# Optimization experiments

Hardware: AMD Instinct MI355X
Metric: run time of the kernel (lower is better)

The kernel has to match this reference:

```python
import jax, jax.numpy as jnp
import numpy as np

B, M, N, D, H = 4, 8, 128, 32, 64
SMALL_V = 1e-8


def setup_inputs() -> dict:
    key = jax.random.key(0)
    ks = jax.random.split(key, 12)
    s = 0.05
    x = jax.random.normal(ks[0], (B, M, N, D), jnp.float32)
    sizes = jax.random.randint(ks[1], (B,), N // 2, N + 1)
    valid = (jnp.arange(N)[None, :] < sizes[:, None]).astype(jnp.float32)  # [B,N]
    x = x * valid[:, None, :, None]  # zero out padded items
    return {
        "x": x,
        "x_size": sizes.astype(jnp.float32),
        "W1a": jax.random.normal(ks[2], (D, 2 * D), jnp.float32) * s,
        "b1a": jax.random.normal(ks[3], (2 * D,), jnp.float32) * s,
        "W1b": jax.random.normal(ks[4], (2 * D, D), jnp.float32) * s,
        "b1b": jax.random.normal(ks[5], (D,), jnp.float32) * s,
        "W2a": jax.random.normal(ks[6], (D, 2 * D), jnp.float32) * s,
        "b2a": jax.random.normal(ks[7], (2 * D,), jnp.float32) * s,
        "W2b": jax.random.normal(ks[8], (2 * D, H), jnp.float32) * s,
        "b2b": jax.random.normal(ks[9], (H,), jnp.float32) * s,
        "w3": jax.random.normal(ks[10], (H,), jnp.float32) * s,
        "b3": jax.random.normal(ks[11], (1,), jnp.float32) * s,
    }


def _item_mask(x):
    # 1.0 where the item's feature row has any nonzero entry, else 0.0. [...,N,1]
    return jnp.any(x != 0, axis=-1, keepdims=True).astype(x.dtype)


def _set_norm(x, x_size):
    # layer_normalization with is_set_norm=True: normalize over (N*D) per set,
    # dividing by the true valid size x_size*D and masking padded items.
    b, m, n, d = x.shape
    mask = jnp.broadcast_to(_item_mask(x), x.shape).reshape(b, m, n * d)
    xr = x.reshape(b, m, n * d)
    denom = x_size[:, None] * d  # [B,1] -> broadcasts over nSet
    mean = jnp.sum(xr, axis=-1) / denom  # [B,M]
    diff = xr - mean[..., None]
    std = jnp.sqrt(jnp.sum(diff * diff * mask, axis=-1) / denom)  # [B,M]
    out = diff / (std[..., None] + SMALL_V) * mask
    return out.reshape(b, m, n, d)


def reference(x, x_size, W1a, b1a, W1b, b1b, W2a, b2a, W2b, b2b, w3, b3):
    mask = _item_mask(x)  # [B,M,N,1]
    x_orig = x
    xn = _set_norm(x, x_size) * mask  # [B,M,N,D]
    # MLP1 (rank-4 -> masked by its own input's item mask)
    m1 = _item_mask(xn)
    x1 = (jnp.matmul(jax.nn.gelu(jnp.matmul(xn, W1a) + b1a), W1b) + b1b) * m1
    # pairwise differences: x_diff[b,m,i,j,:] = x1[b,m,i,:] - xn[b,m,j,:]
    x_diff = x1[:, :, :, None, :] - xn[:, :, None, :, :]  # [B,M,N,N,D]
    # MLP2 (rank-5 -> no mask, is_SoftMax=0)
    e = jnp.matmul(jax.nn.gelu(jnp.matmul(x_diff, W2a) + b2a), W2b) + b2b  # [B,M,N,N,H]
    # aggregation: out[b,m,j,h,d] = sum_i e[b,m,i,j,h] * x1[b,m,i,d]
    agg = jnp.einsum('bmijh,bmid->bmjhd', e, x1)
    # MLP3_linear: Dense(1) over H, then squeeze
    out = jnp.einsum('bmjhd,h->bmjd', agg, w3) + b3[0]
    out = (out + x_orig) * mask
    return out
```

## Files before the change

### kernel.cpp

```cpp
#include <hip/hip_runtime.h>

#define BMC 32
#define NNC 128
#define DDC 32
#define KKC 64
constexpr int ND = NNC * DDC;
constexpr int NK = NNC * KKC;
#define SMALLV 1e-8f

__device__ __forceinline__ float gelu_f(float v) {
    float v2 = v * v;
    float p  = fmaf(0.1029432f, v2, 2.3022082f);
    float e  = __builtin_amdgcn_exp2f(v * p);
    float r  = __builtin_amdgcn_rcpf(e + 1.0f);
    return fmaf(-v, r, v);
}

__global__ __launch_bounds__(256) void mlp_kernel(
    const float* __restrict__ x, const float* __restrict__ x_size,
    const float* __restrict__ W1a, const float* __restrict__ b1a,
    const float* __restrict__ W1b, const float* __restrict__ b1b,
    const float* __restrict__ W2a, const float* __restrict__ b2a,
    const float* __restrict__ W2b, const float* __restrict__ b2b,
    const float* __restrict__ w3,
    float* __restrict__ x1g, float* __restrict__ A1g, float* __restrict__ A2t,
    float* __restrict__ v2g, float* __restrict__ c3g)
{
    __shared__ float sW1a[DDC * KKC];
    __shared__ float sW1b[KKC * DDC];
    __shared__ float sW2a[DDC * KKC];
    __shared__ float sXn[8 * DDC];
    __shared__ float sH[8 * KKC];
    __shared__ float sX1[8 * DDC];
    __shared__ float sB1a[KKC], sB2a[KKC], sB1b[DDC];
    __shared__ float sAny[NNC];
    __shared__ float sRed[4];

    const int t  = threadIdx.x;
    const int bm = blockIdx.x >> 4;
    const int nt = blockIdx.x & 15;
    const int n0 = nt * 8;
    const int w  = t >> 6;

    {
        const float4* a4 = (const float4*)W1a;
        const float4* b4 = (const float4*)W1b;
        const float4* c4 = (const float4*)W2a;
        float4* sa = (float4*)sW1a; float4* sb = (float4*)sW1b; float4* sc = (float4*)sW2a;
        sa[t] = a4[t]; sa[t + 256] = a4[t + 256];
        sb[t] = b4[t]; sb[t + 256] = b4[t + 256];
        sc[t] = c4[t]; sc[t + 256] = c4[t + 256];
    }
    if (t < KKC) { sB1a[t] = b1a[t]; sB2a[t] = b2a[t]; }
    if (t < DDC) { sB1b[t] = b1b[t]; }
    if (t < NNC) sAny[t] = 0.f;
    __syncthreads();

    const float4* xs4 = (const float4*)(x + (size_t)bm * ND);
    float4 v4[4];
    float lsum = 0.f;
    #pragma unroll
    for (int s = 0; s < 4; ++s) {
        int f = t + s * 256;
        float4 q = xs4[f];
        v4[s] = q;
        lsum += q.x + q.y + q.z + q.w;
        if (q.x != 0.f || q.y != 0.f || q.z != 0.f || q.w != 0.f) sAny[f >> 3] = 1.f;
    }
    #pragma unroll
    for (int off = 32; off; off >>= 1) lsum += __shfl_xor(lsum, off);
    if ((t & 63) == 0) sRed[w] = lsum;
    __syncthreads();
    const float denom = x_size[bm >> 3] * (float)DDC;
    const float mean  = (sRed[0] + sRed[1] + sRed[2] + sRed[3]) / denom;

    float lsq = 0.f;
    #pragma unroll
    for (int s = 0; s < 4; ++s) {
        int f = t + s * 256;
        float mk = sAny[f >> 3];
        float dx = v4[s].x - mean, dy = v4[s].y - mean;
        float dz = v4[s].z - mean, dw = v4[s].w - mean;
        lsq += mk * (dx * dx + dy * dy + dz * dz + dw * dw);
    }
    #pragma unroll
    for (int off = 32; off; off >>= 1) lsq += __shfl_xor(lsq, off);
    __syncthreads();
    if ((t & 63) == 0) sRed[w] = lsq;
    __syncthreads();
    const float sq  = sRed[0] + sRed[1] + sRed[2] + sRed[3];
    const float inv = 1.f / (sqrtf(sq / denom) + SMALLV);

    {
        float xv = x[(size_t)bm * ND + n0 * DDC + t];
        sXn[t] = (xv - mean) * inv * sAny[n0 + (t >> 5)];
    }
    __syncthreads();

    const int k = t & 63;

    #pragma unroll
    for (int r = 0; r < 2; ++r) {
        int n = w + r * 4;
        const float* xr = &sXn[n * DDC];
        float acc = sB1a[k];
        #pragma unroll
        for (int d = 0; d < DDC; ++d) acc = fmaf(xr[d], sW1a[d * KKC + k], acc);
        sH[n * KKC + k] = gelu_f(acc);
    }
    __syncthreads();

    {
        const int d2 = t & 31;
        const int n  = t >> 5;
        const float* hr = &sH[n * KKC];
        float acc = sB1b[d2];
        #pragma unroll
        for (int q = 0; q < KKC; ++q) acc = fmaf(hr[q], sW1b[q * DDC + d2], acc);
        float val = acc * sAny[n0 + n];
        sX1[n * DDC + d2] = val;
        x1g[(size_t)bm * ND + (n0 + n) * DDC + d2] = val;
    }
    __syncthreads();

    #pragma unroll
    for (int r = 0; r < 2; ++r) {
        int n = w + r * 4;
        const float* x1r = &sX1[n * DDC];
        const float* xnr = &sXn[n * DDC];
        float a1 = sB2a[k], a2 = 0.f;
        #pragma unroll
        for (int d = 0; d < DDC; ++d) {
            a1 = fmaf(x1r[d], sW2a[d * KKC + k], a1);
            a2 = fmaf(xnr[d], sW2a[d * KKC + k], a2);
        }
        A1g[(size_t)bm * NK + (n0 + n) * KKC + k] = a1;
        A2t[(size_t)bm * NK + k * NNC + (n0 + n)] = a2;
    }

    if (blockIdx.x == 0) {
        int kk = t >> 2, hq = t & 3;
        float p = 0.f;
        #pragma unroll
        for (int h = 0; h < 16; ++h)
            p = fmaf(W2b[kk * KKC + hq * 16 + h], w3[hq * 16 + h], p);
        __syncthreads();
        sH[t] = p;
        __syncthreads();
        if (hq == 0) v2g[kk] = sH[t] + sH[t + 1] + sH[t + 2] + sH[t + 3];
        if (t < 64) {
            float q = b2b[t] * w3[t];
            #pragma unroll
            for (int off = 32; off; off >>= 1) q += __shfl_xor(q, off);
            if (t == 0) c3g[0] = q;
        }
    }
}

__global__ __launch_bounds__(256) void pair_kernel(
    const float* __restrict__ x_size,
    const float* __restrict__ A1g, const float* __restrict__ A2t,
    const float* __restrict__ x1g, const float* __restrict__ v2g,
    const float* __restrict__ c3g, float* __restrict__ partial)
{
    __shared__ float sA2[KKC * 64];
    __shared__ float sA1[8 * KKC];
    __shared__ float sX1[8 * DDC];
    __shared__ float sS[8 * 64];
    __shared__ float sV2[KKC];

    const int t    = threadIdx.x;
    const int bm   = blockIdx.x >> 5;
    const int jg   = (blockIdx.x >> 4) & 1;
    const int ig   = blockIdx.x & 15;

    const int iN = (int)(x_size[bm >> 3] + 0.5f);
    if (ig * 8 >= iN || jg * 64 >= iN) return;

    const int wv   = t >> 6;
    const int lane = t & 63;

    {
        const float* A2b = A2t + (size_t)bm * NK + jg * 64;
        float4* s4 = (float4*)sA2;
        #pragma unroll
        for (int s = 0; s < 4; ++s) {
            int idx = t + s * 256;
            int k = idx >> 4, f = idx & 15;
            s4[idx] = *(const float4*)(A2b + k * NNC + f * 4);
        }
    }
    {
        const float2* a1s = (const float2*)(A1g + (size_t)bm * NK + ig * 8 * KKC);
        ((float2*)sA1)[t] = a1s[t];
        sX1[t] = x1g[(size_t)bm * ND + ig * 8 * DDC + t];
        if (t < KKC) sV2[t] = v2g[t];
    }
    const float c3 = c3g[0];
    __syncthreads();

    {
        const int i0 = wv * 2, i1 = i0 + 1;
        float S0 = c3, S1 = c3;
        #pragma unroll 8
        for (int k = 0; k < KKC; ++k) {
            float a2v = sA2[k * 64 + lane];
            float vk  = sV2[k];
            float a10 = sA1[i0 * KKC + k];
            float a11 = sA1[i1 * KKC + k];
            S0 = fmaf(gelu_f(a10 - a2v), vk, S0);
            S1 = fmaf(gelu_f(a11 - a2v), vk, S1);
        }
        sS[i0 * 64 + lane] = S0;
        sS[i1 * 64 + lane] = S1;
    }
    __syncthreads();

    {
        const int j  = t >> 2;
        const int dq = t & 3;
        float acc[8];
        #pragma unroll
        for (int d = 0; d < 8; ++d) acc[d] = 0.f;
        #pragma unroll
        for (int i = 0; i < 8; ++i) {
            float Sv = sS[i * 64 + j];
            const float4* xf = (const float4*)&sX1[i * DDC + dq * 8];
            float4 xa = xf[0], xb = xf[1];
            acc[0] = fmaf(Sv, xa.x, acc[0]);
            acc[1] = fmaf(Sv, xa.y, acc[1]);
            acc[2] = fmaf(Sv, xa.z, acc[2]);
            acc[3] = fmaf(Sv, xa.w, acc[3]);
            acc[4] = fmaf(Sv, xb.x, acc[4]);
            acc[5] = fmaf(Sv, xb.y, acc[5]);
            acc[6] = fmaf(Sv, xb.z, acc[6]);
            acc[7] = fmaf(Sv, xb.w, acc[7]);
        }
        float* pb = partial + ((size_t)((bm * 2 + jg) * 16 + ig)) * 2048 + t * 8;
        ((float4*)pb)[0] = make_float4(acc[0], acc[1], acc[2], acc[3]);
        ((float4*)pb)[1] = make_float4(acc[4], acc[5], acc[6], acc[7]);
    }
}

__global__ __launch_bounds__(256) void final_kernel(
    const float* __restrict__ x, const float* __restrict__ x_size,
    const float* __restrict__ b3,
    const float* __restrict__ partial, float* __restrict__ out)
{
    const int gid = blockIdx.x * 256 + threadIdx.x;
    const int bm  = gid >> 12;
    const int rem = gid & 4095;
    float xv = x[gid];
    unsigned long long bal = __ballot(xv != 0.f);
    int lane = threadIdx.x & 63;
    unsigned long long half = (lane < 32) ? (bal & 0xFFFFFFFFull) : (bal >> 32);
    if (half == 0ull) { out[gid] = 0.f; return; }

    const int iN  = (int)(x_size[bm >> 3] + 0.5f);
    const int nig = (iN + 7) >> 3;
    const int jgp = rem >> 11;
    const size_t pb = ((size_t)((bm * 2 + jgp) * 16)) * 2048 + (rem & 2047);
    float sum = 0.f;
    for (int ig = 0; ig < nig; ++ig) sum += partial[pb + (size_t)ig * 2048];
    out[gid] = sum + b3[0] + xv;
}

extern "C" void kernel_launch(void* const* d_in, const int* in_sizes, int n_in,
                              void* d_out, int out_size, void* d_ws, size_t ws_size,
                              hipStream_t stream) {
    const float* x      = (const float*)d_in[0];
    const float* x_size = (const float*)d_in[1];
    const float* W1a    = (const float*)d_in[2];
    const float* b1a    = (const float*)d_in[3];
    const float* W1b    = (const float*)d_in[4];
    const float* b1b    = (const float*)d_in[5];
    const float* W2a    = (const float*)d_in[6];
    const float* b2a    = (const float*)d_in[7];
    const float* W2b    = (const float*)d_in[8];
    const float* b2b    = (const float*)d_in[9];
    const float* w3     = (const float*)d_in[10];
    const float* b3     = (const float*)d_in[11];
    float* out = (float*)d_out;

    float* ws      = (float*)d_ws;
    float* x1g     = ws;
    float* A1g     = x1g + (size_t)BMC * ND;
    float* A2t     = A1g + (size_t)BMC * NK;
    float* v2g     = A2t + (size_t)BMC * NK;
    float* c3g     = v2g + KKC;
    float* partial = c3g + 64;

    mlp_kernel<<<BMC * 16, 256, 0, stream>>>(x, x_size,
        W1a, b1a, W1b, b1b, W2a, b2a, W2b, b2b, w3,
        x1g, A1g, A2t, v2g, c3g);
    pair_kernel<<<BMC * 32, 256, 0, stream>>>(x_size, A1g, A2t, x1g, v2g, c3g, partial);
    final_kernel<<<512, 256, 0, stream>>>(x, x_size, b3, partial, out);
}
```

Baseline: 104.0 us.

## Fuse final reduction into pair kernel via atomics and register-cache A2 tiles

Removes the separate final reduction kernel: the MLP kernel now seeds the output with x+b3 (zero for padded rows), and the pair kernel atomically adds its per-i-group contributions straight into the output. The pair kernel also handles 16 source items per block, caches each thread's A2 column in registers and computes four rows per wave with vectorized shared loads. This removes a launch and the partial buffer round trip, at the cost of global atomics and higher register pressure. The padding mask now comes from x_size instead of nonzero rows.

New measurement: 122.7 us. 1.18x slower.

```diff
diff --git a/kernel.cpp b/kernel.cpp
--- a/kernel.cpp
+++ b/kernel.cpp
@@ -22,9 +22,9 @@
     const float* __restrict__ W1b, const float* __restrict__ b1b,
     const float* __restrict__ W2a, const float* __restrict__ b2a,
     const float* __restrict__ W2b, const float* __restrict__ b2b,
-    const float* __restrict__ w3,
+    const float* __restrict__ w3, const float* __restrict__ b3,
     float* __restrict__ x1g, float* __restrict__ A1g, float* __restrict__ A2t,
-    float* __restrict__ v2g, float* __restrict__ c3g)
+    float* __restrict__ v2g, float* __restrict__ c3g, float* __restrict__ out)
 {
     __shared__ float sW1a[DDC * KKC];
     __shared__ float sW1b[KKC * DDC];
@@ -71,7 +71,9 @@
     for (int off = 32; off; off >>= 1) lsum += __shfl_xor(lsum, off);
     if ((t & 63) == 0) sRed[w] = lsum;
     __syncthreads();
-    const float denom = x_size[bm >> 3] * (float)DDC;
+    const float xsz   = x_size[bm >> 3];
+    const float denom = xsz * (float)DDC;
+    const int   iN    = (int)(xsz + 0.5f);
     const float mean  = (sRed[0] + sRed[1] + sRed[2] + sRed[3]) / denom;
 
     float lsq = 0.f;
@@ -93,7 +95,9 @@
 
     {
         float xv = x[(size_t)bm * ND + n0 * DDC + t];
-        sXn[t] = (xv - mean) * inv * sAny[n0 + (t >> 5)];
+        int  jr  = n0 + (t >> 5);
+        sXn[t] = (xv - mean) * inv * sAny[jr];
+        out[(size_t)bm * ND + n0 * DDC + t] = (jr < iN) ? xv + b3[0] : 0.f;
     }
     __syncthreads();
 
@@ -161,21 +165,21 @@
     const float* __restrict__ x_size,
     const float* __restrict__ A1g, const float* __restrict__ A2t,
     const float* __restrict__ x1g, const float* __restrict__ v2g,
-    const float* __restrict__ c3g, float* __restrict__ partial)
+    const float* __restrict__ c3g, float* __restrict__ out)
 {
     __shared__ float sA2[KKC * 64];
-    __shared__ float sA1[8 * KKC];
-    __shared__ float sX1[8 * DDC];
-    __shared__ float sS[8 * 64];
+    __shared__ float sA1[16 * KKC];
+    __shared__ float sX1[16 * DDC];
+    __shared__ float sS[16 * 64];
     __shared__ float sV2[KKC];
 
     const int t    = threadIdx.x;
-    const int bm   = blockIdx.x >> 5;
-    const int jg   = (blockIdx.x >> 4) & 1;
-    const int ig   = blockIdx.x & 15;
+    const int bm   = blockIdx.x >> 4;
+    const int jg   = (blockIdx.x >> 3) & 1;
+    const int ig   = blockIdx.x & 7;
 
     const int iN = (int)(x_size[bm >> 3] + 0.5f);
-    if (ig * 8 >= iN || jg * 64 >= iN) return;
+    if (ig * 16 >= iN || jg * 64 >= iN) return;
 
     const int wv   = t >> 6;
     const int lane = t & 63;
@@ -190,29 +194,53 @@
             s4[idx] = *(const float4*)(A2b + k * NNC + f * 4);
         }
     }
-    {
-        const float2* a1s = (const float2*)(A1g + (size_t)bm * NK + ig * 8 * KKC);
-        ((float2*)sA1)[t] = a1s[t];
-        sX1[t] = x1g[(size_t)bm * ND + ig * 8 * DDC + t];
-        if (t < KKC) sV2[t] = v2g[t];
-    }
+    ((float4*)sA1)[t] = ((const float4*)(A1g + (size_t)bm * NK + ig * 16 * KKC))[t];
+    ((float2*)sX1)[t] = ((const float2*)(x1g + (size_t)bm * ND + ig * 16 * DDC))[t];
+    if (t < KKC) sV2[t] = v2g[t];
     const float c3 = c3g[0];
     __syncthreads();
 
-    {
-        const int i0 = wv * 2, i1 = i0 + 1;
-        float S0 = c3, S1 = c3;
-        #pragma unroll 8
-        for (int k = 0; k < KKC; ++k) {
-            float a2v = sA2[k * 64 + lane];
-            float vk  = sV2[k];
-            float a10 = sA1[i0 * KKC + k];
-            float a11 = sA1[i1 * KKC + k];
-            S0 = fmaf(gelu_f(a10 - a2v), vk, S0);
-            S1 = fmaf(gelu_f(a11 - a2v), vk, S1);
-        }
-        sS[i0 * 64 + lane] = S0;
-        sS[i1 * 64 + lane] = S1;
+    float a2r[KKC];
+    #pragma unroll
+    for (int q = 0; q < KKC; ++q) a2r[q] = sA2[q * 64 + lane];
+
+    {
+        const float4* a1f0 = (const float4*)&sA1[(wv * 4 + 0) * KKC];
+        const float4* a1f1 = (const float4*)&sA1[(wv * 4 + 1) * KKC];
+        const float4* a1f2 = (const float4*)&sA1[(wv * 4 + 2) * KKC];
+        const float4* a1f3 = (const float4*)&sA1[(wv * 4 + 3) * KKC];
+        const float4* v2f  = (const float4*)sV2;
+        float S0 = c3, S1 = c3, S2 = c3, S3 = c3;
+        #pragma unroll 4
+        for (int k4 = 0; k4 < 16; ++k4) {
+            float4 vk = v2f[k4];
+            float4 a0 = a1f0[k4];
+            float4 a1 = a1f1[k4];
+            float4 a2 = a1f2[k4];
+            float4 a3 = a1f3[k4];
+            const int kb = k4 * 4;
+            float b0 = a2r[kb + 0], b1 = a2r[kb + 1], b2 = a2r[kb + 2], b3v = a2r[kb + 3];
+            S0 = fmaf(gelu_f(a0.x - b0), vk.x, S0);
+            S1 = fmaf(gelu_f(a1.x - b0), vk.x, S1);
+            S2 = fmaf(gelu_f(a2.x - b0), vk.x, S2);
+            S3 = fmaf(gelu_f(a3.x - b0), vk.x, S3);
+            S0 = fmaf(gelu_f(a0.y - b1), vk.y, S0);
+            S1 = fmaf(gelu_f(a1.y - b1), vk.y, S1);
+            S2 = fmaf(gelu_f(a2.y - b1), vk.y, S2);
+            S3 = fmaf(gelu_f(a3.y - b1), vk.y, S3);
+            S0 = fmaf(gelu_f(a0.z - b2), vk.z, S0);
+            S1 = fmaf(gelu_f(a1.z - b2), vk.z, S1);
+            S2 = fmaf(gelu_f(a2.z - b2), vk.z, S2);
+            S3 = fmaf(gelu_f(a3.z - b2), vk.z, S3);
+            S0 = fmaf(gelu_f(a0.w - b3v), vk.w, S0);
+            S1 = fmaf(gelu_f(a1.w - b3v), vk.w, S1);
+            S2 = fmaf(gelu_f(a2.w - b3v), vk.w, S2);
+            S3 = fmaf(gelu_f(a3.w - b3v), vk.w, S3);
+        }
+        sS[(wv * 4 + 0) * 64 + lane] = S0;
+        sS[(wv * 4 + 1) * 64 + lane] = S1;
+        sS[(wv * 4 + 2) * 64 + lane] = S2;
+        sS[(wv * 4 + 3) * 64 + lane] = S3;
     }
     __syncthreads();
 
@@ -223,7 +251,7 @@
         #pragma unroll
         for (int d = 0; d < 8; ++d) acc[d] = 0.f;
         #pragma unroll
-        for (int i = 0; i < 8; ++i) {
+        for (int i = 0; i < 16; ++i) {
             float Sv = sS[i * 64 + j];
             const float4* xf = (const float4*)&sX1[i * DDC + dq * 8];
             float4 xa = xf[0], xb = xf[1];
@@ -236,33 +264,13 @@
             acc[6] = fmaf(Sv, xb.z, acc[6]);
             acc[7] = fmaf(Sv, xb.w, acc[7]);
         }
-        float* pb = partial + ((size_t)((bm * 2 + jg) * 16 + ig)) * 2048 + t * 8;
-        ((float4*)pb)[0] = make_float4(acc[0], acc[1], acc[2], acc[3]);
-        ((float4*)pb)[1] = make_float4(acc[4], acc[5], acc[6], acc[7]);
-    }
-}
-
-__global__ __launch_bounds__(256) void final_kernel(
-    const float* __restrict__ x, const float* __restrict__ x_size,
-    const float* __restrict__ b3,
-    const float* __restrict__ partial, float* __restrict__ out)
-{
-    const int gid = blockIdx.x * 256 + threadIdx.x;
-    const int bm  = gid >> 12;
-    const int rem = gid & 4095;
-    float xv = x[gid];
-    unsigned long long bal = __ballot(xv != 0.f);
-    int lane = threadIdx.x & 63;
-    unsigned long long half = (lane < 32) ? (bal & 0xFFFFFFFFull) : (bal >> 32);
-    if (half == 0ull) { out[gid] = 0.f; return; }
-
-    const int iN  = (int)(x_size[bm >> 3] + 0.5f);
-    const int nig = (iN + 7) >> 3;
-    const int jgp = rem >> 11;
-    const size_t pb = ((size_t)((bm * 2 + jgp) * 16)) * 2048 + (rem & 2047);
-    float sum = 0.f;
-    for (int ig = 0; ig < nig; ++ig) sum += partial[pb + (size_t)ig * 2048];
-    out[gid] = sum + b3[0] + xv;
+        const int jglob = jg * 64 + j;
+        if (jglob < iN) {
+            float* ob = out + (size_t)bm * ND + jglob * DDC + dq * 8;
+            #pragma unroll
+            for (int q = 0; q < 8; ++q) atomicAdd(ob + q, acc[q]);
+        }
+    }
 }
 
 extern "C" void kernel_launch(void* const* d_in, const int* in_sizes, int n_in,
@@ -282,17 +290,15 @@
     const float* b3     = (const float*)d_in[11];
     float* out = (float*)d_out;
 
-    float* ws      = (float*)d_ws;
-    float* x1g     = ws;
-    float* A1g     = x1g + (size_t)BMC * ND;
-    float* A2t     = A1g + (size_t)BMC * NK;
-    float* v2g     = A2t + (size_t)BMC * NK;
-    float* c3g     = v2g + KKC;
-    float* partial = c3g + 64;
+    float* ws  = (float*)d_ws;
+    float* x1g = ws;
+    float* A1g = x1g + (size_t)BMC * ND;
+    float* A2t = A1g + (size_t)BMC * NK;
+    float* v2g = A2t + (size_t)BMC * NK;
+    float* c3g = v2g + KKC;
 
     mlp_kernel<<<BMC * 16, 256, 0, stream>>>(x, x_size,
-        W1a, b1a, W1b, b1b, W2a, b2a, W2b, b2b, w3,
-        x1g, A1g, A2t, v2g, c3g);
-    pair_kernel<<<BMC * 32, 256, 0, stream>>>(x_size, A1g, A2t, x1g, v2g, c3g, partial);
-    final_kernel<<<512, 256, 0, stream>>>(x, x_size, b3, partial, out);
+        W1a, b1a, W1b, b1b, W2a, b2a, W2b, b2b, w3, b3,
+        x1g, A1g, A2t, v2g, c3g, out);
+    pair_kernel<<<BMC * 16, 256, 0, stream>>>(x_size, A1g, A2t, x1g, v2g, c3g, out);
 }
```

## Split pair kernel into score and aggregation kernels with row-major A2

Applied to the files above, without the earlier changes.

Stores A2 row-major so each lane loads its 64 k-values straight into registers instead of staging a transposed tile in LDS. The pair kernel now writes the full score matrix S to global memory, and the final kernel performs the i-sum aggregation directly over valid items rather than reducing per-tile partials. This removes the in-block aggregation step, its barriers and LDS use, and allows higher occupancy, at the cost of a larger score buffer and strided global reads in the aggregation. The output mask now uses j < x_size instead of the per-item nonzero check.

New measurement: 113.1 us. +8.7%, slower.

```diff
diff --git a/kernel.cpp b/kernel.cpp
--- a/kernel.cpp
+++ b/kernel.cpp
@@ -6,6 +6,7 @@
 #define KKC 64
 constexpr int ND = NNC * DDC;
 constexpr int NK = NNC * KKC;
+constexpr int NS = NNC * NNC;
 #define SMALLV 1e-8f
 
 __device__ __forceinline__ float gelu_f(float v) {
@@ -23,7 +24,7 @@
     const float* __restrict__ W2a, const float* __restrict__ b2a,
     const float* __restrict__ W2b, const float* __restrict__ b2b,
     const float* __restrict__ w3,
-    float* __restrict__ x1g, float* __restrict__ A1g, float* __restrict__ A2t,
+    float* __restrict__ x1g, float* __restrict__ A1g, float* __restrict__ A2r,
     float* __restrict__ v2g, float* __restrict__ c3g)
 {
     __shared__ float sW1a[DDC * KKC];
@@ -71,7 +72,8 @@
     for (int off = 32; off; off >>= 1) lsum += __shfl_xor(lsum, off);
     if ((t & 63) == 0) sRed[w] = lsum;
     __syncthreads();
-    const float denom = x_size[bm >> 3] * (float)DDC;
+    const float xsz   = x_size[bm >> 3];
+    const float denom = xsz * (float)DDC;
     const float mean  = (sRed[0] + sRed[1] + sRed[2] + sRed[3]) / denom;
 
     float lsq = 0.f;
@@ -135,7 +137,7 @@
             a2 = fmaf(xnr[d], sW2a[d * KKC + k], a2);
         }
         A1g[(size_t)bm * NK + (n0 + n) * KKC + k] = a1;
-        A2t[(size_t)bm * NK + k * NNC + (n0 + n)] = a2;
+        A2r[(size_t)bm * NK + (n0 + n) * KKC + k] = a2;
     }
 
     if (blockIdx.x == 0) {
@@ -157,22 +159,19 @@
     }
 }
 
-__global__ __launch_bounds__(256) void pair_kernel(
+__global__ __launch_bounds__(256, 4) void score_kernel(
     const float* __restrict__ x_size,
-    const float* __restrict__ A1g, const float* __restrict__ A2t,
-    const float* __restrict__ x1g, const float* __restrict__ v2g,
-    const float* __restrict__ c3g, float* __restrict__ partial)
+    const float* __restrict__ A1g, const float* __restrict__ A2r,
+    const float* __restrict__ v2g, const float* __restrict__ c3g,
+    float* __restrict__ Sg)
 {
-    __shared__ float sA2[KKC * 64];
     __shared__ float sA1[8 * KKC];
-    __shared__ float sX1[8 * DDC];
-    __shared__ float sS[8 * 64];
     __shared__ float sV2[KKC];
 
-    const int t    = threadIdx.x;
-    const int bm   = blockIdx.x >> 5;
-    const int jg   = (blockIdx.x >> 4) & 1;
-    const int ig   = blockIdx.x & 15;
+    const int t  = threadIdx.x;
+    const int bm = blockIdx.x >> 5;
+    const int jg = (blockIdx.x >> 4) & 1;
+    const int ig = blockIdx.x & 15;
 
     const int iN = (int)(x_size[bm >> 3] + 0.5f);
     if (ig * 8 >= iN || jg * 64 >= iN) return;
@@ -180,89 +179,67 @@
     const int wv   = t >> 6;
     const int lane = t & 63;
 
-    {
-        const float* A2b = A2t + (size_t)bm * NK + jg * 64;
-        float4* s4 = (float4*)sA2;
-        #pragma unroll
-        for (int s = 0; s < 4; ++s) {
-            int idx = t + s * 256;
-            int k = idx >> 4, f = idx & 15;
-            s4[idx] = *(const float4*)(A2b + k * NNC + f * 4);
-        }
-    }
-    {
-        const float2* a1s = (const float2*)(A1g + (size_t)bm * NK + ig * 8 * KKC);
-        ((float2*)sA1)[t] = a1s[t];
-        sX1[t] = x1g[(size_t)bm * ND + ig * 8 * DDC + t];
-        if (t < KKC) sV2[t] = v2g[t];
-    }
+    ((float2*)sA1)[t] = ((const float2*)(A1g + (size_t)bm * NK + ig * 8 * KKC))[t];
+    if (t < KKC) sV2[t] = v2g[t];
     const float c3 = c3g[0];
-    __syncthreads();
-
-    {
-        const int i0 = wv * 2, i1 = i0 + 1;
-        float S0 = c3, S1 = c3;
-        #pragma unroll 8
-        for (int k = 0; k < KKC; ++k) {
-            float a2v = sA2[k * 64 + lane];
-            float vk  = sV2[k];
-            float a10 = sA1[i0 * KKC + k];
-            float a11 = sA1[i1 * KKC + k];
-            S0 = fmaf(gelu_f(a10 - a2v), vk, S0);
-            S1 = fmaf(gelu_f(a11 - a2v), vk, S1);
-        }
-        sS[i0 * 64 + lane] = S0;
-        sS[i1 * 64 + lane] = S1;
-    }
-    __syncthreads();
-
-    {
-        const int j  = t >> 2;
-        const int dq = t & 3;
-        float acc[8];
-        #pragma unroll
-        for (int d = 0; d < 8; ++d) acc[d] = 0.f;
-        #pragma unroll
-        for (int i = 0; i < 8; ++i) {
-            float Sv = sS[i * 64 + j];
-            const float4* xf = (const float4*)&sX1[i * DDC + dq * 8];
-            float4 xa = xf[0], xb = xf[1];
-            acc[0] = fmaf(Sv, xa.x, acc[0]);
-            acc[1] = fmaf(Sv, xa.y, acc[1]);
-            acc[2] = fmaf(Sv, xa.z, acc[2]);
-            acc[3] = fmaf(Sv, xa.w, acc[3]);
-            acc[4] = fmaf(Sv, xb.x, acc[4]);
-            acc[5] = fmaf(Sv, xb.y, acc[5]);
-            acc[6] = fmaf(Sv, xb.z, acc[6]);
-            acc[7] = fmaf(Sv, xb.w, acc[7]);
-        }
-        float* pb = partial + ((size_t)((bm * 2 + jg) * 16 + ig)) * 2048 + t * 8;
-        ((float4*)pb)[0] = make_float4(acc[0], acc[1], acc[2], acc[3]);
-        ((float4*)pb)[1] = make_float4(acc[4], acc[5], acc[6], acc[7]);
-    }
-}
-
-__global__ __launch_bounds__(256) void final_kernel(
+
+    const float4* a2p = (const float4*)(A2r + (size_t)bm * NK + (jg * 64 + lane) * KKC);
+    float4 a2q[16];
+    #pragma unroll
+    for (int q = 0; q < 16; ++q) a2q[q] = a2p[q];
+    __syncthreads();
+
+    const float4* a1f0 = (const float4*)&sA1[(wv * 2 + 0) * KKC];
+    const float4* a1f1 = (const float4*)&sA1[(wv * 2 + 1) * KKC];
+    const float4* v2f  = (const float4*)sV2;
+
+    float S0 = c3, S1 = c3;
+    #pragma unroll
+    for (int q = 0; q < 16; ++q) {
+        float4 a0 = a1f0[q];
+        float4 a1 = a1f1[q];
+        float4 vv = v2f[q];
+        float4 b  = a2q[q];
+        S0 = fmaf(gelu_f(a0.x - b.x), vv.x, S0);
+        S1 = fmaf(gelu_f(a1.x - b.x), vv.x, S1);
+        S0 = fmaf(gelu_f(a0.y - b.y), vv.y, S0);
+        S1 = fmaf(gelu_f(a1.y - b.y), vv.y, S1);
+        S0 = fmaf(gelu_f(a0.z - b.z), vv.z, S0);
+        S1 = fmaf(gelu_f(a1.z - b.z), vv.z, S1);
+        S0 = fmaf(gelu_f(a0.w - b.w), vv.w, S0);
+        S1 = fmaf(gelu_f(a1.w - b.w), vv.w, S1);
+    }
+    const int i0 = ig * 8 + wv * 2;
+    const int jc = jg * 64 + lane;
+    Sg[(size_t)bm * NS + (i0 + 0) * NNC + jc] = S0;
+    Sg[(size_t)bm * NS + (i0 + 1) * NNC + jc] = S1;
+}
+
+__global__ __launch_bounds__(256) void agg_kernel(
     const float* __restrict__ x, const float* __restrict__ x_size,
     const float* __restrict__ b3,
-    const float* __restrict__ partial, float* __restrict__ out)
+    const float* __restrict__ Sg, const float* __restrict__ x1g,
+    float* __restrict__ out)
 {
     const int gid = blockIdx.x * 256 + threadIdx.x;
     const int bm  = gid >> 12;
-    const int rem = gid & 4095;
-    float xv = x[gid];
-    unsigned long long bal = __ballot(xv != 0.f);
-    int lane = threadIdx.x & 63;
-    unsigned long long half = (lane < 32) ? (bal & 0xFFFFFFFFull) : (bal >> 32);
-    if (half == 0ull) { out[gid] = 0.f; return; }
-
+    const int d   = gid & 31;
+    const int j   = (gid >> 5) & 127;
     const int iN  = (int)(x_size[bm >> 3] + 0.5f);
-    const int nig = (iN + 7) >> 3;
-    const int jgp = rem >> 11;
-    const size_t pb = ((size_t)((bm * 2 + jgp) * 16)) * 2048 + (rem & 2047);
-    float sum = 0.f;
-    for (int ig = 0; ig < nig; ++ig) sum += partial[pb + (size_t)ig * 2048];
-    out[gid] = sum + b3[0] + xv;
+    if (j >= iN) { out[gid] = 0.f; return; }
+
+    const float* Sp = Sg + (size_t)bm * NS + j;
+    const float* xp = x1g + (size_t)bm * ND + d;
+    float a0 = 0.f, a1 = 0.f, a2 = 0.f, a3 = 0.f;
+    int i = 0;
+    for (; i + 4 <= iN; i += 4) {
+        a0 = fmaf(Sp[(i + 0) * NNC], xp[(i + 0) * DDC], a0);
+        a1 = fmaf(Sp[(i + 1) * NNC], xp[(i + 1) * DDC], a1);
+        a2 = fmaf(Sp[(i + 2) * NNC], xp[(i + 2) * DDC], a2);
+        a3 = fmaf(Sp[(i + 3) * NNC], xp[(i + 3) * DDC], a3);
+    }
+    for (; i < iN; ++i) a0 = fmaf(Sp[i * NNC], xp[i * DDC], a0);
+    out[gid] = (a0 + a1) + (a2 + a3) + b3[0] + x[gid];
 }
 
 extern "C" void kernel_launch(void* const* d_in, const int* in_sizes, int n_in,
@@ -282,17 +259,17 @@
     const float* b3     = (const float*)d_in[11];
     float* out = (float*)d_out;
 
-    float* ws      = (float*)d_ws;
-    float* x1g     = ws;
-    float* A1g     = x1g + (size_t)BMC * ND;
-    float* A2t     = A1g + (size_t)BMC * NK;
-    float* v2g     = A2t + (size_t)BMC * NK;
-    float* c3g     = v2g + KKC;
-    float* partial = c3g + 64;
+    float* ws  = (float*)d_ws;
+    float* x1g = ws;
+    float* A1g = x1g + (size_t)BMC * ND;
+    float* A2r = A1g + (size_t)BMC * NK;
+    float* v2g = A2r + (size_t)BMC * NK;
+    float* c3g = v2g + KKC;
+    float* Sg  = c3g + 64;
 
     mlp_kernel<<<BMC * 16, 256, 0, stream>>>(x, x_size,
         W1a, b1a, W1b, b1b, W2a, b2a, W2b, b2b, w3,
-        x1g, A1g, A2t, v2g, c3g);
-    pair_kernel<<<BMC * 32, 256, 0, stream>>>(x_size, A1g, A2t, x1g, v2g, c3g, partial);
-    final_kernel<<<512, 256, 0, stream>>>(x, x_size, b3, partial, out);
-}
+        x1g, A1g, A2r, v2g, c3g);
+    score_kernel<<<BMC * 32, 256, 0, stream>>>(x_size, A1g, A2r, v2g, c3g, Sg);
+    agg_kernel<<<512, 256, 0, stream>>>(x, x_size, b3, Sg, x1g, out);
+}
```
